# Performance work log

Hardware: AMD Instinct MI355X
Metric: run time of the kernel (lower is better)

Reference implementation:

```python
import jax, jax.numpy as jnp
import numpy as np

D = 128
EPS = 1e-3
B, S = 16, 512
N_TRI = (D - 1) * D // 2


def _build_lu(lower_entries, upper_entries, unconstrained_upper_diag):
    li = jnp.tril_indices(D, k=-1)
    ui = jnp.triu_indices(D, k=1)
    di = jnp.diag_indices(D)
    lower = jnp.zeros((D, D), dtype=lower_entries.dtype)
    lower = lower.at[li].set(lower_entries).at[di].set(1.0)
    upper_diag = jax.nn.softplus(unconstrained_upper_diag) + EPS
    upper = jnp.zeros((D, D), dtype=upper_entries.dtype)
    upper = upper.at[ui].set(upper_entries).at[di].set(upper_diag)
    return lower, upper


def setup_inputs() -> dict:
    key = jax.random.key(0)
    ks = jax.random.split(key, 6)
    return {
        "x": jax.random.normal(ks[0], (B, S, D), dtype=jnp.float32),
        "mask": jax.random.randint(ks[1], (B, S, D), 0, 2, dtype=jnp.int32),
        "lower_entries": jax.random.normal(ks[2], (N_TRI,), dtype=jnp.float32),
        "upper_entries": jax.random.normal(ks[3], (N_TRI,), dtype=jnp.float32),
        "unconstrained_upper_diag": jax.random.normal(ks[4], (D,), dtype=jnp.float32),
        "bias": jax.random.normal(ks[5], (D,), dtype=jnp.float32),
    }


def reference(x, mask, lower_entries, upper_entries, unconstrained_upper_diag, bias):
    b = x.shape[0]
    d = x.shape[-1]
    x2 = x.reshape(-1, d)                      # [n, d], n = b*s
    m = mask.reshape(-1, d)                    # [n, d] int
    mb = m.astype(bool)

    lower, upper = _build_lu(lower_entries, upper_entries, unconstrained_upper_diag)

    # masked rows/cols of L and U replaced by identity rows/cols
    mm = mb[:, :, None] & mb[:, None, :]       # [n, d, d]
    eye = jnp.eye(d, dtype=x2.dtype)
    upper_b = jnp.where(mm, upper, eye)        # [n, d, d]
    lower_b = jnp.where(mm, lower, eye)        # [n, d, d]
    bias_b = bias * m.astype(x2.dtype)         # [n, d]

    log_det = jnp.sum(jnp.log(jnp.diagonal(upper_b, axis1=-2, axis2=-1)), axis=-1)  # [n]

    y = jnp.einsum('bij,bj->bi', upper_b, x2)
    y = jnp.einsum('bij,bj->bi', lower_b, y) + bias_b

    y = y.reshape(b, -1, d)
    log_det = log_det.reshape(b, -1)
    return y, log_det, mask


if __name__ == "__main__":
    out = reference(**setup_inputs())
    print(out[0].shape, out[1].shape)
```

## Files before the change

kernel.cpp:

```cpp
#include <hip/hip_runtime.h>

#define D 128
#define EPS 1e-3f

typedef short short8v __attribute__((ext_vector_type(8)));
typedef float f32x4  __attribute__((ext_vector_type(4)));
typedef unsigned short u16;
typedef u16 u16x4 __attribute__((ext_vector_type(4)));

#define U_OFF 0
#define L_OFF (32*1024)
#define LD_OFF (64*1024)

__device__ __forceinline__ float softplus_f(float x) {
    return (x > 20.f) ? x : log1pf(expf(x));
}
__device__ __forceinline__ u16 f2bf(float f) {
    unsigned u = __float_as_uint(f);
    unsigned r = (u + 0x7FFFu + ((u >> 16) & 1u)) >> 16;
    return (u16)r;
}

__global__ __launch_bounds__(256)
void lu_setup_kernel(const float* __restrict__ low_e,
                     const float* __restrict__ up_e,
                     const float* __restrict__ ud,
                     char* __restrict__ ws)
{
    const int wc = blockIdx.x;
    const int s  = threadIdx.x >> 6;
    const int l  = threadIdx.x & 63;
    const int i  = wc * 16 + (l & 15);
    const int k0 = s * 32 + (l >> 4) * 8;

    short8v uv8, lv8;
    #pragma unroll
    for (int e = 0; e < 8; ++e) {
        const int j = k0 + e;
        float uvf, lvf;
        if (j > i)      { uvf = up_e[i * 127 - (i * (i - 1)) / 2 + (j - i - 1)]; lvf = 0.f; }
        else if (j < i) { uvf = 0.f; lvf = low_e[(i * (i - 1)) / 2 + j]; }
        else            { uvf = softplus_f(ud[i]) + EPS; lvf = 1.f; }
        uv8[e] = (short)f2bf(uvf);
        lv8[e] = (short)f2bf(lvf);
    }
    const int fidx = (wc * 4 + s) * 64 + l;
    *((short8v*)(ws + U_OFF) + fidx) = uv8;
    *((short8v*)(ws + L_OFF) + fidx) = lv8;

    if (blockIdx.x == 0 && threadIdx.x < D) {
        const float dg = softplus_f(ud[threadIdx.x]) + EPS;
        ((float*)(ws + LD_OFF))[threadIdx.x] = logf(dg);
    }
}

__global__ __launch_bounds__(512, 2)
void lu_mfma_kernel(const float* __restrict__ x,
                    const int*   __restrict__ mask,
                    const float* __restrict__ bias,
                    const char*  __restrict__ ws,
                    float* __restrict__ out_y,
                    float* __restrict__ out_logdet,
                    float* __restrict__ out_mask)
{
    __shared__ u16   xm_lds[16 * 128];
    __shared__ float x_lds[16 * 132];
    __shared__ u16   m_lds[16 * 132];

    const int t    = threadIdx.x;
    const int w    = t >> 6;
    const int l    = t & 63;
    const int row0 = blockIdx.x * 16;

    short8v ufrag[4], lfrag[4];
    #pragma unroll
    for (int s = 0; s < 4; ++s) {
        const int fidx = (w * 4 + s) * 64 + l;
        ufrag[s] = *((const short8v*)(ws + U_OFF) + fidx);
        lfrag[s] = *((const short8v*)(ws + L_OFF) + fidx);
    }

    const int srow = t >> 5;
    const int c0   = (t & 31) * 4;
    const float4 xv = *(const float4*)(x    + (size_t)(row0 + srow) * D + c0);
    const int4   mv = *(const int4*)  (mask + (size_t)(row0 + srow) * D + c0);

    *(float4*)(out_mask + (size_t)(row0 + srow) * D + c0) =
        make_float4((float)mv.x, (float)mv.y, (float)mv.z, (float)mv.w);

    *(float4*)&x_lds[srow * 132 + c0] = xv;
    u16x4 mq; mq[0]=(u16)mv.x; mq[1]=(u16)mv.y; mq[2]=(u16)mv.z; mq[3]=(u16)mv.w;
    *(u16x4*)&m_lds[srow * 132 + c0] = mq;

    u16x4 xb;
    xb[0] = f2bf(mv.x ? xv.x : 0.f);
    xb[1] = f2bf(mv.y ? xv.y : 0.f);
    xb[2] = f2bf(mv.z ? xv.z : 0.f);
    xb[3] = f2bf(mv.w ? xv.w : 0.f);
    const int xi = (srow * 128 + c0) ^ ((srow & 7) << 3);
    *(u16x4*)&xm_lds[xi] = xb;

    const float4 ldg = *(const float4*)((const float*)(ws + LD_OFF) + c0);
    float part = (mv.x ? ldg.x : 0.f) + (mv.y ? ldg.y : 0.f) +
                 (mv.z ? ldg.z : 0.f) + (mv.w ? ldg.w : 0.f);
    #pragma unroll
    for (int sh = 16; sh > 0; sh >>= 1) part += __shfl_xor(part, sh, 64);
    if ((t & 31) == 0) out_logdet[row0 + srow] = part;

    __syncthreads();

    const int arow = l & 15;
    const int ablk = (l >> 4) * 8;
    f32x4 acc = {0.f, 0.f, 0.f, 0.f};
    #pragma unroll
    for (int s = 0; s < 4; ++s) {
        const int ai = (arow * 128 + s * 32 + ablk) ^ ((arow & 7) << 3);
        const short8v a = *(const short8v*)&xm_lds[ai];
        acc = __builtin_amdgcn_mfma_f32_16x16x32_bf16(a, ufrag[s], acc, 0, 0, 0);
    }

    __syncthreads();

    const int ccol = 16 * w + (l & 15);
    #pragma unroll
    for (int p = 0; p < 4; ++p) {
        const int r = (l >> 4) * 4 + p;
        const u16 m = m_lds[r * 132 + ccol];
        const float v = m ? acc[p] : 0.f;
        const int yi = (r * 128 + ccol) ^ ((r & 7) << 3);
        xm_lds[yi] = f2bf(v);
    }

    __syncthreads();

    f32x4 acc2 = {0.f, 0.f, 0.f, 0.f};
    #pragma unroll
    for (int s = 0; s < 4; ++s) {
        const int ai = (arow * 128 + s * 32 + ablk) ^ ((arow & 7) << 3);
        const short8v a = *(const short8v*)&xm_lds[ai];
        acc2 = __builtin_amdgcn_mfma_f32_16x16x32_bf16(a, lfrag[s], acc2, 0, 0, 0);
    }

    const float bv = bias[ccol];
    #pragma unroll
    for (int p = 0; p < 4; ++p) {
        const int r = (l >> 4) * 4 + p;
        const u16 m = m_lds[r * 132 + ccol];
        const float yv = m ? (acc2[p] + bv) : x_lds[r * 132 + ccol];
        out_y[(size_t)(row0 + r) * D + ccol] = yv;
    }
}

extern "C" void kernel_launch(void* const* d_in, const int* in_sizes, int n_in,
                              void* d_out, int out_size, void* d_ws, size_t ws_size,
                              hipStream_t stream) {
    const float* x     = (const float*)d_in[0];
    const int*   mask  = (const int*)d_in[1];
    const float* low_e = (const float*)d_in[2];
    const float* up_e  = (const float*)d_in[3];
    const float* ud    = (const float*)d_in[4];
    const float* bias  = (const float*)d_in[5];

    const int n_rows = in_sizes[0] / D;
    float* out_y      = (float*)d_out;
    float* out_logdet = out_y + (size_t)n_rows * D;
    float* out_mask   = out_logdet + n_rows;

    char* ws = (char*)d_ws;

    lu_setup_kernel<<<8, 256, 0, stream>>>(low_e, up_e, ud, ws);
    lu_mfma_kernel<<<n_rows / 16, 512, 0, stream>>>(
        x, mask, bias, ws, out_y, out_logdet, out_mask);
}
```

Baseline: 73.99 us.

## Fuse LU matrix setup into main MFMA kernel, dropping setup launch

Removes the separate setup kernel and its workspace. Each block now builds its own bf16 U and L fragments straight from the packed triangular parameter arrays, using a packed bf16 convert instruction, and recomputes the log-diagonal terms locally. This saves one kernel launch and the serial dependency between the two kernels. In exchange, every one of the 512 blocks does redundant gathers of the triangular entries plus softplus/log math. The launch-bounds occupancy hint is also raised from 2 to 4.

```diff
diff --git a/kernel.cpp b/kernel.cpp
--- a/kernel.cpp
+++ b/kernel.cpp
@@ -8,10 +8,6 @@
 typedef unsigned short u16;
 typedef u16 u16x4 __attribute__((ext_vector_type(4)));
 
-#define U_OFF 0
-#define L_OFF (32*1024)
-#define LD_OFF (64*1024)
-
 __device__ __forceinline__ float softplus_f(float x) {
     return (x > 20.f) ? x : log1pf(expf(x));
 }
@@ -20,48 +16,22 @@
     unsigned r = (u + 0x7FFFu + ((u >> 16) & 1u)) >> 16;
     return (u16)r;
 }
+__device__ __forceinline__ unsigned cvt_pk_bf16(float lo, float hi) {
+    unsigned r;
+    asm("v_cvt_pk_bf16_f32 %0, %1, %2" : "=v"(r) : "v"(lo), "v"(hi));
+    return r;
+}
 
-__global__ __launch_bounds__(256)
-void lu_setup_kernel(const float* __restrict__ low_e,
+__global__ __launch_bounds__(512, 4)
+void lu_fused_kernel(const float* __restrict__ x,
+                     const int*   __restrict__ mask,
+                     const float* __restrict__ low_e,
                      const float* __restrict__ up_e,
                      const float* __restrict__ ud,
-                     char* __restrict__ ws)
-{
-    const int wc = blockIdx.x;
-    const int s  = threadIdx.x >> 6;
-    const int l  = threadIdx.x & 63;
-    const int i  = wc * 16 + (l & 15);
-    const int k0 = s * 32 + (l >> 4) * 8;
-
-    short8v uv8, lv8;
-    #pragma unroll
-    for (int e = 0; e < 8; ++e) {
-        const int j = k0 + e;
-        float uvf, lvf;
-        if (j > i)      { uvf = up_e[i * 127 - (i * (i - 1)) / 2 + (j - i - 1)]; lvf = 0.f; }
-        else if (j < i) { uvf = 0.f; lvf = low_e[(i * (i - 1)) / 2 + j]; }
-        else            { uvf = softplus_f(ud[i]) + EPS; lvf = 1.f; }
-        uv8[e] = (short)f2bf(uvf);
-        lv8[e] = (short)f2bf(lvf);
-    }
-    const int fidx = (wc * 4 + s) * 64 + l;
-    *((short8v*)(ws + U_OFF) + fidx) = uv8;
-    *((short8v*)(ws + L_OFF) + fidx) = lv8;
-
-    if (blockIdx.x == 0 && threadIdx.x < D) {
-        const float dg = softplus_f(ud[threadIdx.x]) + EPS;
-        ((float*)(ws + LD_OFF))[threadIdx.x] = logf(dg);
-    }
-}
-
-__global__ __launch_bounds__(512, 2)
-void lu_mfma_kernel(const float* __restrict__ x,
-                    const int*   __restrict__ mask,
-                    const float* __restrict__ bias,
-                    const char*  __restrict__ ws,
-                    float* __restrict__ out_y,
-                    float* __restrict__ out_logdet,
-                    float* __restrict__ out_mask)
+                     const float* __restrict__ bias,
+                     float* __restrict__ out_y,
+                     float* __restrict__ out_logdet,
+                     float* __restrict__ out_mask)
 {
     __shared__ u16   xm_lds[16 * 128];
     __shared__ float x_lds[16 * 132];
@@ -72,18 +42,47 @@
     const int l    = t & 63;
     const int row0 = blockIdx.x * 16;
 
-    short8v ufrag[4], lfrag[4];
-    #pragma unroll
-    for (int s = 0; s < 4; ++s) {
-        const int fidx = (w * 4 + s) * 64 + l;
-        ufrag[s] = *((const short8v*)(ws + U_OFF) + fidx);
-        lfrag[s] = *((const short8v*)(ws + L_OFF) + fidx);
-    }
-
     const int srow = t >> 5;
     const int c0   = (t & 31) * 4;
     const float4 xv = *(const float4*)(x    + (size_t)(row0 + srow) * D + c0);
     const int4   mv = *(const int4*)  (mask + (size_t)(row0 + srow) * D + c0);
+
+    const int i  = w * 16 + (l & 15);
+    const int kb = (l >> 4) * 8;
+    const float dgi = softplus_f(ud[i]) + EPS;
+    const int ubase = i * 127 - (i * (i - 1)) / 2 - i - 1;
+    const int lbase = (i * (i - 1)) / 2;
+
+    short8v ufrag[4], lfrag[4];
+    #pragma unroll
+    for (int s = 0; s < 4; ++s) {
+        float uf[8], lf[8];
+        #pragma unroll
+        for (int e = 0; e < 8; ++e) {
+            const int j  = s * 32 + kb + e;
+            const int ui = (j > i) ? (ubase + j) : 0;
+            const int li = (j < i) ? (lbase + j) : 0;
+            const float uv = up_e[ui];
+            const float lv = low_e[li];
+            uf[e] = (j > i) ? uv : ((j == i) ? dgi : 0.f);
+            lf[e] = (j < i) ? lv : ((j == i) ? 1.f : 0.f);
+        }
+        union { short8v s8; unsigned u[4]; } uu, llu;
+        #pragma unroll
+        for (int h = 0; h < 4; ++h) {
+            uu.u[h]  = cvt_pk_bf16(uf[2*h], uf[2*h+1]);
+            llu.u[h] = cvt_pk_bf16(lf[2*h], lf[2*h+1]);
+        }
+        ufrag[s] = uu.s8;
+        lfrag[s] = llu.s8;
+    }
+    const float bv = bias[i];
+
+    const f32x4 udv = *(const f32x4*)(ud + c0);
+    const float ld0 = logf(softplus_f(udv[0]) + EPS);
+    const float ld1 = logf(softplus_f(udv[1]) + EPS);
+    const float ld2 = logf(softplus_f(udv[2]) + EPS);
+    const float ld3 = logf(softplus_f(udv[3]) + EPS);
 
     *(float4*)(out_mask + (size_t)(row0 + srow) * D + c0) =
         make_float4((float)mv.x, (float)mv.y, (float)mv.z, (float)mv.w);
@@ -100,9 +99,8 @@
     const int xi = (srow * 128 + c0) ^ ((srow & 7) << 3);
     *(u16x4*)&xm_lds[xi] = xb;
 
-    const float4 ldg = *(const float4*)((const float*)(ws + LD_OFF) + c0);
-    float part = (mv.x ? ldg.x : 0.f) + (mv.y ? ldg.y : 0.f) +
-                 (mv.z ? ldg.z : 0.f) + (mv.w ? ldg.w : 0.f);
+    float part = (mv.x ? ld0 : 0.f) + (mv.y ? ld1 : 0.f) +
+                 (mv.z ? ld2 : 0.f) + (mv.w ? ld3 : 0.f);
     #pragma unroll
     for (int sh = 16; sh > 0; sh >>= 1) part += __shfl_xor(part, sh, 64);
     if ((t & 31) == 0) out_logdet[row0 + srow] = part;
@@ -121,13 +119,12 @@
 
     __syncthreads();
 
-    const int ccol = 16 * w + (l & 15);
     #pragma unroll
     for (int p = 0; p < 4; ++p) {
         const int r = (l >> 4) * 4 + p;
-        const u16 m = m_lds[r * 132 + ccol];
+        const u16 m = m_lds[r * 132 + i];
         const float v = m ? acc[p] : 0.f;
-        const int yi = (r * 128 + ccol) ^ ((r & 7) << 3);
+        const int yi = (r * 128 + i) ^ ((r & 7) << 3);
         xm_lds[yi] = f2bf(v);
     }
 
@@ -141,13 +138,12 @@
         acc2 = __builtin_amdgcn_mfma_f32_16x16x32_bf16(a, lfrag[s], acc2, 0, 0, 0);
     }
 
-    const float bv = bias[ccol];
     #pragma unroll
     for (int p = 0; p < 4; ++p) {
         const int r = (l >> 4) * 4 + p;
-        const u16 m = m_lds[r * 132 + ccol];
-        const float yv = m ? (acc2[p] + bv) : x_lds[r * 132 + ccol];
-        out_y[(size_t)(row0 + r) * D + ccol] = yv;
+        const u16 m = m_lds[r * 132 + i];
+        const float yv = m ? (acc2[p] + bv) : x_lds[r * 132 + i];
+        out_y[(size_t)(row0 + r) * D + i] = yv;
     }
 }
 
@@ -166,9 +162,6 @@
     float* out_logdet = out_y + (size_t)n_rows * D;
     float* out_mask   = out_logdet + n_rows;
 
-    char* ws = (char*)d_ws;
-
-    lu_setup_kernel<<<8, 256, 0, stream>>>(low_e, up_e, ud, ws);
-    lu_mfma_kernel<<<n_rows / 16, 512, 0, stream>>>(
-        x, mask, bias, ws, out_y, out_logdet, out_mask);
+    lu_fused_kernel<<<n_rows / 16, 512, 0, stream>>>(
+        x, mask, low_e, up_e, ud, bias, out_y, out_logdet, out_mask);
 }
```

Result: slower. 78.83 us (+6.5%).
